# Performance work log

Hardware: AMD Instinct MI355X
Metric: run time of the kernel (lower is better)

## Reference

```python
import jax, jax.numpy as jnp
import numpy as np

B, D, N, M, R, C = 512, 16, 64, 32, 32, 10  # batch, divisions, feat_in, feat_map, TR-rank, categories


def setup_inputs() -> dict:
    key = jax.random.key(0)
    k1, k2, k3, k4 = jax.random.split(key, 4)
    tensor = jax.random.normal(k1, (B, D, N), dtype=jnp.float32)
    W_fm = jax.random.normal(k2, (N, M), dtype=jnp.float32) / np.sqrt(N)
    b_fm = jax.random.normal(k3, (M,), dtype=jnp.float32) * 0.01
    # one [R, M, R] tensor-ring core per (category, division)
    G = jax.random.normal(k4, (C, D, R, M, R), dtype=jnp.float32) / np.sqrt(M * R)
    return {"tensor": tensor, "W_fm": W_fm, "b_fm": b_fm, "G": G}


def reference(tensor, W_fm, b_fm, G):
    # FeatureMap: learned linear n -> m applied per division  [B, D, M]
    feat = jnp.einsum('bdn,nm->bdm', tensor, W_fm) + b_fm
    # CoreKernelTensorRing per (category, division): [B,M] x [R,M,R] -> [B,R,R]
    cores = jnp.einsum('bdm,cdimj->cdbij', feat, G)  # [C, D, B, R, R]
    # __foward_products: chained batched matmul along divisions (structural loop, D fixed)
    prod = cores[:, 0]  # [C, B, R, R]
    for d in range(1, D):
        prod = jnp.matmul(prod, cores[:, d])
    # __calculate_traces: per-sample trace, one logit per category
    logits = jnp.einsum('cbii->bc', prod)  # [B, C]
    return jax.nn.log_softmax(logits, axis=1)
```

## Files before the change

### kernel.cpp

```cpp
#include <hip/hip_runtime.h>
#include <math.h>

#define BB 512
#define DD 16
#define NN 64
#define MM 32
#define RR 32
#define CC 10
#define ISTR 40
#define BSTR 1288

typedef _Float16 v8h __attribute__((ext_vector_type(8)));
typedef float v4f __attribute__((ext_vector_type(4)));
typedef float v16f __attribute__((ext_vector_type(16)));

union H8 { unsigned int u[4]; v8h h; _Float16 e[8]; };
union H4 { unsigned int u[2]; _Float16 e[4]; };

__device__ inline unsigned pk2(float a, float b) {
    union { unsigned u; _Float16 e[2]; } v;
    v.e[0] = (_Float16)a; v.e[1] = (_Float16)b;
    return v.u;
}

__global__ __launch_bounds__(256) void produce_kernel(
    const float* __restrict__ tensor, const float* __restrict__ W,
    const float* __restrict__ bias,   const float* __restrict__ G,
    _Float16* __restrict__ fh,        _Float16* __restrict__ gh) {
    __shared__ __align__(16) char smem[36864];
    const int t = threadIdx.x;
    if (blockIdx.x < 1024) {
        float* ten_s = (float*)smem;
        float* W_s   = (float*)smem + 512;
        const int bd0 = blockIdx.x * 8;
        if (t < 128)
            *(float4*)(ten_s + t * 4) = *(const float4*)(tensor + bd0 * NN + t * 4);
        *(float4*)(W_s + t * 4)        = *(const float4*)(W + t * 4);
        *(float4*)(W_s + 1024 + t * 4) = *(const float4*)(W + 1024 + t * 4);
        __syncthreads();
        const int m = t & 31, bd_l = t >> 5;
        float acc = bias[m];
#pragma unroll
        for (int n = 0; n < NN; ++n) acc += ten_s[bd_l * NN + n] * W_s[n * MM + m];
        fh[(bd0 + bd_l) * MM + m] = (_Float16)acc;
    } else {
        _Float16* lg = (_Float16*)smem;
        const int pb = blockIdx.x - 1024;
        const int c  = pb >> 5;
        const int d  = (pb >> 1) & 15;
        const int hf = pb & 1;
        const float* src = G + (size_t)(c * DD + d) * 32768 + hf * 16384;
#pragma unroll
        for (int k = 0; k < 16; ++k) {
            const int f = (k * 256 + t) * 4;
            float4 v = *(const float4*)(src + f);
            const int di = f >> 10, m = (f >> 5) & 31, j = f & 31;
            H4 hv;
            hv.e[0] = (_Float16)v.x; hv.e[1] = (_Float16)v.y;
            hv.e[2] = (_Float16)v.z; hv.e[3] = (_Float16)v.w;
            *(uint2*)(lg + di * 1152 + m * 36 + j) = make_uint2(hv.u[0], hv.u[1]);
        }
        __syncthreads();
#pragma unroll
        for (int k = 0; k < 8; ++k) {
            const int idx = k * 256 + t;
            const int tl = idx >> 6, ln = idx & 63;
            const int di = tl >> 1, ks = tl & 1;
            const int hh = ln >> 5, j = ln & 31;
            H8 o;
#pragma unroll
            for (int r = 0; r < 8; ++r)
                o.e[r] = lg[di * 1152 + (16 * ks + 8 * hh + r) * 36 + j];
            const size_t gi = ((size_t)(c * DD + d) * 64 + hf * 32 + tl) * 64 + ln;
            *(v8h*)(gh + gi * 8) = o.h;
        }
    }
}

__global__ __launch_bounds__(512, 2) void chain_kernel(
    const _Float16* __restrict__ feat_h,
    const _Float16* __restrict__ g_h,
    float* __restrict__ trout)
{
    __shared__ __align__(16) _Float16 lds[32 * BSTR];

    const int bid = blockIdx.x;
    const int xcd = bid & 7;
    const int idx = bid >> 3;
    int c, sub;
    if (idx < 16) { c = xcd; sub = idx; }
    else {
        const int e = idx - 16;
        c = 8 + (xcd >> 2);
        sub = (xcd & 3) * 4 + e;
    }
    const int b0 = sub * 32;
    const int t    = threadIdx.x;
    const int w    = t >> 6;
    const int lane = t & 63;
    const int h    = lane >> 5;
    const int col  = lane & 31;

    const int wp4 = 4 * ((w & 4) | ((w & 1) << 1) | ((w & 2) >> 1));

    const size_t gc = (size_t)c * DD * 32768;
    const _Float16* fb = feat_h + (size_t)(b0 + col) * (DD * MM);

    const v16f z16 = {0.f,0.f,0.f,0.f,0.f,0.f,0.f,0.f,
                      0.f,0.f,0.f,0.f,0.f,0.f,0.f,0.f};

    v8h af[2];
#pragma unroll
    for (int ks = 0; ks < 2; ++ks)
        af[ks] = *(const v8h*)(fb + 16 * ks + 8 * h);
    v8h gB[4][2];
#pragma unroll
    for (int il = 0; il < 4; ++il)
#pragma unroll
        for (int ks = 0; ks < 2; ++ks)
            gB[il][ks] = *(const v8h*)(g_h + gc +
                ((size_t)(((4 * w + il) * 2 + ks) * 64) + lane) * 8);

    v8h sb[4][2];
    {
        H8 x0, x1;
#pragma unroll
        for (int r = 0; r < 8; ++r) {
            const int pi = (r & 3) + 8 * (r >> 2) + 4 * h;
            x0.e[r] = (_Float16)((pi == col) ? 1.0f : 0.0f);
            x1.e[r] = (_Float16)((pi + 16 == col) ? 1.0f : 0.0f);
        }
#pragma unroll
        for (int cc = 0; cc < 4; ++cc) { sb[cc][0] = x0.h; sb[cc][1] = x1.h; }
    }

    for (int d = 0; d < DD; ++d) {
        __syncthreads();
        v16f av[4];
#pragma unroll
        for (int il = 0; il < 4; ++il) {
            av[il] = __builtin_amdgcn_mfma_f32_32x32x16_f16(af[0], gB[il][0], z16, 0, 0, 0);
            av[il] = __builtin_amdgcn_mfma_f32_32x32x16_f16(af[1], gB[il][1], av[il], 0, 0, 0);
        }
        if (d < DD - 1) {
#pragma unroll
            for (int ks = 0; ks < 2; ++ks)
                af[ks] = *(const v8h*)(fb + (d + 1) * MM + 16 * ks + 8 * h);
            const size_t gb = gc + (size_t)(d + 1) * 32768;
#pragma unroll
            for (int il = 0; il < 4; ++il)
#pragma unroll
                for (int ks = 0; ks < 2; ++ks)
                    gB[il][ks] = *(const v8h*)(g_h + gb +
                        ((size_t)(((4 * w + il) * 2 + ks) * 64) + lane) * 8);
        }
#pragma unroll
        for (int r16 = 0; r16 < 16; ++r16) {
            const int b = (r16 & 3) + 8 * (r16 >> 2) + 4 * h;
            H4 hv;
            hv.e[0] = (_Float16)av[0][r16];
            hv.e[1] = (_Float16)av[1][r16];
            hv.e[2] = (_Float16)av[2][r16];
            hv.e[3] = (_Float16)av[3][r16];
            *(uint2*)(lds + b * BSTR + col * ISTR + wp4) =
                make_uint2(hv.u[0], hv.u[1]);
        }
        __syncthreads();
#pragma unroll
        for (int cc = 0; cc < 4; ++cc) {
            _Float16* base = lds + (4 * w + cc) * BSTR;
            v8h a0 = *(const v8h*)(base + col * ISTR + 8 * h);
            v8h a1 = *(const v8h*)(base + col * ISTR + 16 + 8 * h);
            v16f acc;
            acc = __builtin_amdgcn_mfma_f32_32x32x16_f16(a0, sb[cc][0], z16, 0, 0, 0);
            acc = __builtin_amdgcn_mfma_f32_32x32x16_f16(a1, sb[cc][1], acc, 0, 0, 0);
            if (d == DD - 1) {
                float ts = 0.f;
#pragma unroll
                for (int r16 = 0; r16 < 16; ++r16) {
                    const int row = (r16 & 3) + 8 * (r16 >> 2) + 4 * h;
                    if (row == col) ts += acc[r16];
                }
#pragma unroll
                for (int off = 32; off > 0; off >>= 1)
                    ts += __shfl_xor(ts, off);
                if (lane == 0)
                    trout[(size_t)(b0 + 4 * w + cc) * CC + c] = ts;
            } else {
                H8 s0, s1;
                s0.u[0] = pk2(acc[0],  acc[1]);
                s0.u[1] = pk2(acc[2],  acc[3]);
                s0.u[2] = pk2(acc[4],  acc[5]);
                s0.u[3] = pk2(acc[6],  acc[7]);
                s1.u[0] = pk2(acc[8],  acc[9]);
                s1.u[1] = pk2(acc[10], acc[11]);
                s1.u[2] = pk2(acc[12], acc[13]);
                s1.u[3] = pk2(acc[14], acc[15]);
                sb[cc][0] = s0.h;
                sb[cc][1] = s1.h;
            }
        }
    }
}

__global__ __launch_bounds__(256) void lsm_kernel(
    const float* __restrict__ tr, float* __restrict__ out) {
    const int b = blockIdx.x * 256 + threadIdx.x;
    float v[CC];
    float mx = -1e30f;
#pragma unroll
    for (int c = 0; c < CC; ++c) {
        v[c] = tr[b * CC + c];
        mx = fmaxf(mx, v[c]);
    }
    float ssum = 0.f;
#pragma unroll
    for (int c = 0; c < CC; ++c) ssum += expf(v[c] - mx);
    const float ls = logf(ssum);
#pragma unroll
    for (int c = 0; c < CC; ++c) out[b * CC + c] = v[c] - mx - ls;
}

extern "C" void kernel_launch(void* const* d_in, const int* in_sizes, int n_in,
                              void* d_out, int out_size, void* d_ws, size_t ws_size,
                              hipStream_t stream) {
    const float* tensor = (const float*)d_in[0];
    const float* W      = (const float*)d_in[1];
    const float* bias   = (const float*)d_in[2];
    const float* G      = (const float*)d_in[3];
    float* out = (float*)d_out;

    const size_t FEAT = (size_t)BB * DD * MM;
    const size_t GPK  = (size_t)CC * DD * 64 * 64 * 8;
    _Float16* fh = (_Float16*)d_ws;
    _Float16* gh = fh + FEAT;
    float* trbuf = (float*)(gh + GPK);

    produce_kernel<<<1024 + 320, 256, 0, stream>>>(tensor, W, bias, G, fh, gh);
    chain_kernel<<<160, 512, 0, stream>>>(fh, gh, trbuf);
    lsm_kernel<<<BB / 256, 256, 0, stream>>>(trbuf, out);
}
```

Baseline: 116.6 us.

## Split division chain into two halves per block and combine via trace of product

The 16-division matrix chain is split into two 8-step halves, each computed by separate blocks over 16-sample batches, so the grid grows from 160 to 640 blocks with half the LDS each. Each half writes its partial 32x32 product to global memory in fp16, with the second half stored transposed. A new combine kernel computes trace(P0*P1) as an elementwise dot product and then applies log-softmax. This adds more parallelism and occupancy on a latency-bound serial chain, at the cost of extra global traffic for the partial matrices and an extra fp16 rounding of them.

```diff
diff --git a/kernel.cpp b/kernel.cpp
--- a/kernel.cpp
+++ b/kernel.cpp
@@ -77,24 +77,27 @@
     }
 }
 
-__global__ __launch_bounds__(512, 2) void chain_kernel(
+__global__ __launch_bounds__(512, 4) void chain_kernel(
     const _Float16* __restrict__ feat_h,
     const _Float16* __restrict__ g_h,
-    float* __restrict__ trout)
+    _Float16* __restrict__ mbuf)
 {
-    __shared__ __align__(16) _Float16 lds[32 * BSTR];
+    __shared__ __align__(16) _Float16 lds[16 * BSTR];
 
     const int bid = blockIdx.x;
     const int xcd = bid & 7;
     const int idx = bid >> 3;
-    int c, sub;
-    if (idx < 16) { c = xcd; sub = idx; }
+    int c, unit;
+    if (idx < 64) { c = xcd; unit = idx; }
     else {
-        const int e = idx - 16;
+        const int e = idx - 64;
         c = 8 + (xcd >> 2);
-        sub = (xcd & 3) * 4 + e;
-    }
-    const int b0 = sub * 32;
+        unit = (xcd & 3) * 16 + e;
+    }
+    const int s   = unit & 1;
+    const int sub = unit >> 1;
+    const int b0  = sub * 16;
+
     const int t    = threadIdx.x;
     const int w    = t >> 6;
     const int lane = t & 63;
@@ -104,24 +107,26 @@
     const int wp4 = 4 * ((w & 4) | ((w & 1) << 1) | ((w & 2) >> 1));
 
     const size_t gc = (size_t)c * DD * 32768;
-    const _Float16* fb = feat_h + (size_t)(b0 + col) * (DD * MM);
+    const _Float16* fb = feat_h + (size_t)(b0 + (col & 15)) * (DD * MM);
 
     const v16f z16 = {0.f,0.f,0.f,0.f,0.f,0.f,0.f,0.f,
                       0.f,0.f,0.f,0.f,0.f,0.f,0.f,0.f};
 
+    const int d0 = 8 * s;
+
     v8h af[2];
 #pragma unroll
     for (int ks = 0; ks < 2; ++ks)
-        af[ks] = *(const v8h*)(fb + 16 * ks + 8 * h);
+        af[ks] = *(const v8h*)(fb + d0 * MM + 16 * ks + 8 * h);
     v8h gB[4][2];
 #pragma unroll
     for (int il = 0; il < 4; ++il)
 #pragma unroll
         for (int ks = 0; ks < 2; ++ks)
-            gB[il][ks] = *(const v8h*)(g_h + gc +
+            gB[il][ks] = *(const v8h*)(g_h + gc + (size_t)d0 * 32768 +
                 ((size_t)(((4 * w + il) * 2 + ks) * 64) + lane) * 8);
 
-    v8h sb[4][2];
+    v8h sb[2][2];
     {
         H8 x0, x1;
 #pragma unroll
@@ -131,10 +136,11 @@
             x1.e[r] = (_Float16)((pi + 16 == col) ? 1.0f : 0.0f);
         }
 #pragma unroll
-        for (int cc = 0; cc < 4; ++cc) { sb[cc][0] = x0.h; sb[cc][1] = x1.h; }
-    }
-
-    for (int d = 0; d < DD; ++d) {
+        for (int cc = 0; cc < 2; ++cc) { sb[cc][0] = x0.h; sb[cc][1] = x1.h; }
+    }
+
+    for (int dd = 0; dd < 8; ++dd) {
+        const int d = d0 + dd;
         __syncthreads();
         v16f av[4];
 #pragma unroll
@@ -142,7 +148,7 @@
             av[il] = __builtin_amdgcn_mfma_f32_32x32x16_f16(af[0], gB[il][0], z16, 0, 0, 0);
             av[il] = __builtin_amdgcn_mfma_f32_32x32x16_f16(af[1], gB[il][1], av[il], 0, 0, 0);
         }
-        if (d < DD - 1) {
+        if (dd < 7) {
 #pragma unroll
             for (int ks = 0; ks < 2; ++ks)
                 af[ks] = *(const v8h*)(fb + (d + 1) * MM + 16 * ks + 8 * h);
@@ -155,7 +161,7 @@
                         ((size_t)(((4 * w + il) * 2 + ks) * 64) + lane) * 8);
         }
 #pragma unroll
-        for (int r16 = 0; r16 < 16; ++r16) {
+        for (int r16 = 0; r16 < 8; ++r16) {
             const int b = (r16 & 3) + 8 * (r16 >> 2) + 4 * h;
             H4 hv;
             hv.e[0] = (_Float16)av[0][r16];
@@ -167,25 +173,38 @@
         }
         __syncthreads();
 #pragma unroll
-        for (int cc = 0; cc < 4; ++cc) {
-            _Float16* base = lds + (4 * w + cc) * BSTR;
+        for (int cc = 0; cc < 2; ++cc) {
+            _Float16* base = lds + (2 * w + cc) * BSTR;
             v8h a0 = *(const v8h*)(base + col * ISTR + 8 * h);
             v8h a1 = *(const v8h*)(base + col * ISTR + 16 + 8 * h);
             v16f acc;
             acc = __builtin_amdgcn_mfma_f32_32x32x16_f16(a0, sb[cc][0], z16, 0, 0, 0);
             acc = __builtin_amdgcn_mfma_f32_32x32x16_f16(a1, sb[cc][1], acc, 0, 0, 0);
-            if (d == DD - 1) {
-                float ts = 0.f;
-#pragma unroll
-                for (int r16 = 0; r16 < 16; ++r16) {
-                    const int row = (r16 & 3) + 8 * (r16 >> 2) + 4 * h;
-                    if (row == col) ts += acc[r16];
+            if (dd == 7) {
+                if (s == 0) {
+#pragma unroll
+                    for (int g = 0; g < 4; ++g) {
+                        const unsigned lo = pk2(acc[4 * g + 0], acc[4 * g + 1]);
+                        const unsigned hi = pk2(acc[4 * g + 2], acc[4 * g + 3]);
+                        *(uint2*)(base + col * 32 + 8 * g + 4 * h) =
+                            make_uint2(lo, hi);
+                    }
+                } else {
+#pragma unroll
+                    for (int r16 = 0; r16 < 16; ++r16) {
+                        const int row = (r16 & 3) + 8 * (r16 >> 2) + 4 * h;
+                        base[row * 32 + col] = (_Float16)acc[r16];
+                    }
                 }
-#pragma unroll
-                for (int off = 32; off > 0; off >>= 1)
-                    ts += __shfl_xor(ts, off);
-                if (lane == 0)
-                    trout[(size_t)(b0 + 4 * w + cc) * CC + c] = ts;
+                __builtin_amdgcn_sched_barrier(0);
+                asm volatile("s_waitcnt lgkmcnt(0)" ::: "memory");
+                __builtin_amdgcn_sched_barrier(0);
+                const v8h mlo = *(const v8h*)(base + lane * 16);
+                const v8h mhi = *(const v8h*)(base + lane * 16 + 8);
+                _Float16* mb = mbuf + ((((size_t)s * CC + c) * 32 + sub) * 16 +
+                                       (2 * w + cc)) * 1024;
+                *(v8h*)(mb + lane * 16)     = mlo;
+                *(v8h*)(mb + lane * 16 + 8) = mhi;
             } else {
                 H8 s0, s1;
                 s0.u[0] = pk2(acc[0],  acc[1]);
@@ -203,22 +222,43 @@
     }
 }
 
-__global__ __launch_bounds__(256) void lsm_kernel(
-    const float* __restrict__ tr, float* __restrict__ out) {
-    const int b = blockIdx.x * 256 + threadIdx.x;
-    float v[CC];
+__global__ __launch_bounds__(128) void combine_lsm_kernel(
+    const _Float16* __restrict__ mbuf, float* __restrict__ out) {
+    const int t    = threadIdx.x;
+    const int b    = blockIdx.x * 2 + (t >> 6);
+    const int lane = t & 63;
+
+    float tr[CC];
+#pragma unroll
+    for (int c = 0; c < CC; ++c) {
+        const _Float16* p0 = mbuf +
+            (((size_t)c * 32 + (b >> 4)) * 16 + (b & 15)) * 1024 + lane * 16;
+        const _Float16* p1 = mbuf +
+            ((((size_t)CC + c) * 32 + (b >> 4)) * 16 + (b & 15)) * 1024 + lane * 16;
+        v8h x0 = ((const v8h*)p0)[0];
+        v8h x1 = ((const v8h*)p0)[1];
+        v8h y0 = ((const v8h*)p1)[0];
+        v8h y1 = ((const v8h*)p1)[1];
+        float acc = 0.f;
+#pragma unroll
+        for (int e = 0; e < 8; ++e)
+            acc += (float)x0[e] * (float)y0[e] + (float)x1[e] * (float)y1[e];
+#pragma unroll
+        for (int off = 32; off > 0; off >>= 1)
+            acc += __shfl_xor(acc, off);
+        tr[c] = acc;
+    }
     float mx = -1e30f;
 #pragma unroll
-    for (int c = 0; c < CC; ++c) {
-        v[c] = tr[b * CC + c];
-        mx = fmaxf(mx, v[c]);
-    }
+    for (int c = 0; c < CC; ++c) mx = fmaxf(mx, tr[c]);
     float ssum = 0.f;
 #pragma unroll
-    for (int c = 0; c < CC; ++c) ssum += expf(v[c] - mx);
+    for (int c = 0; c < CC; ++c) ssum += expf(tr[c] - mx);
     const float ls = logf(ssum);
-#pragma unroll
-    for (int c = 0; c < CC; ++c) out[b * CC + c] = v[c] - mx - ls;
+    float val = 0.f;
+#pragma unroll
+    for (int c = 0; c < CC; ++c) if (lane == c) val = tr[c] - mx - ls;
+    if (lane < CC) out[b * CC + lane] = val;
 }
 
 extern "C" void kernel_launch(void* const* d_in, const int* in_sizes, int n_in,
@@ -232,11 +272,11 @@
 
     const size_t FEAT = (size_t)BB * DD * MM;
     const size_t GPK  = (size_t)CC * DD * 64 * 64 * 8;
-    _Float16* fh = (_Float16*)d_ws;
-    _Float16* gh = fh + FEAT;
-    float* trbuf = (float*)(gh + GPK);
+    _Float16* fh   = (_Float16*)d_ws;
+    _Float16* gh   = fh + FEAT;
+    _Float16* mbuf = gh + GPK;
 
     produce_kernel<<<1024 + 320, 256, 0, stream>>>(tensor, W, bias, G, fh, gh);
-    chain_kernel<<<160, 512, 0, stream>>>(fh, gh, trbuf);
-    lsm_kernel<<<BB / 256, 256, 0, stream>>>(trbuf, out);
-}
+    chain_kernel<<<640, 512, 0, stream>>>(fh, gh, mbuf);
+    combine_lsm_kernel<<<BB / 2, 128, 0, stream>>>(mbuf, out);
+}
```

After: 111.2 us, median of 2. 4.7% less time.
